# Performance work log

Hardware: AMD Instinct MI355X
Metric: run time of the kernel (lower is better)

The kernel has to match this reference:

```python
import jax, jax.numpy as jnp
import numpy as np

MAXDISP = 48


def setup_inputs() -> dict:
    key = jax.random.key(0)
    k1, k2 = jax.random.split(key)
    B, C, H, W = 4, 32, 64, 128
    x = jax.random.normal(k1, (B, C, H, W), dtype=jnp.float32)
    y = jax.random.normal(k2, (B, C, H, W), dtype=jnp.float32)
    return {"x": x, "y": y}


def reference(x, y):
    # cost[b, :C, d, h, w]   = x[b, :, h, w]     if w >= d else 0
    # cost[b, C:, d, h, w]   = y[b, :, h, w - d] if w >= d else 0
    B, C, H, W = x.shape
    D = MAXDISP
    d = jnp.arange(D)[:, None]            # [D, 1]
    w = jnp.arange(W)[None, :]            # [1, W]
    mask = (w >= d)                       # [D, W]
    mask_b = mask[None, None, :, None, :] # [1, 1, D, 1, W]

    # left features: broadcast over D, mask out w < d
    x_part = jnp.where(mask_b, x[:, :, None, :, :], 0.0)  # [B, C, D, H, W]

    # right features: gather shifted columns w - d (clipped), then mask
    y_idx = jnp.maximum(w - d, 0)                         # [D, W]
    y_g = jnp.take(y, y_idx, axis=3)                      # [B, C, H, D, W]
    y_g = jnp.transpose(y_g, (0, 1, 3, 2, 4))             # [B, C, D, H, W]
    y_part = jnp.where(mask_b, y_g, 0.0)

    return jnp.concatenate([x_part, y_part], axis=1)      # [B, 2C, D, H, W]
```

## Files before the change

### kernel.cpp

```cpp
#include <hip/hip_runtime.h>


#define CV_DSTRIDE (64 * 32)

__global__ __launch_bounds__(256) void cost_volume_kernel(
    const float* __restrict__ x, const float* __restrict__ y,
    float4* __restrict__ out)
{
    const int tid = blockIdx.x * 256 + threadIdx.x;
    const int w4 = tid & 31;
    const int h  = (tid >> 5) & 63;
    const int cc = (tid >> 11) & 63;
    const int b  = tid >> 17;
    const int w0 = w4 * 4;

    float4* outp = out + (((((b * 64 + cc) * 48) * 64 + h) * 32) + w4);

#define STORE_D(dv, e0, e1, e2, e3)                        \
    {                                                      \
        const int d_ = (dv);                               \
        float4 v;                                          \
        v.x = (w0 + 0 >= d_) ? (e0) : 0.0f;                \
        v.y = (w0 + 1 >= d_) ? (e1) : 0.0f;                \
        v.z = (w0 + 2 >= d_) ? (e2) : 0.0f;                \
        v.w = (w0 + 3 >= d_) ? (e3) : 0.0f;                \
        outp[d_ * CV_DSTRIDE] = v;                         \
    }

    if (cc < 32) {
        const float4 xv =
            *(const float4*)(x + ((b * 32 + cc) * 64 + h) * 128 + w0);
#pragma unroll
        for (int d = 0; d < 48; ++d) {
            STORE_D(d, xv.x, xv.y, xv.z, xv.w);
        }
    } else {
        float4 cur =
            *(const float4*)(y + ((b * 32 + (cc - 32)) * 64 + h) * 128 + w0);
#pragma unroll
        for (int q = 0; q < 12; ++q) {
            float4 prev;
            prev.x = __shfl_up(cur.x, 1, 32);
            prev.y = __shfl_up(cur.y, 1, 32);
            prev.z = __shfl_up(cur.z, 1, 32);
            prev.w = __shfl_up(cur.w, 1, 32);
            STORE_D(4 * q + 0, cur.x,  cur.y,  cur.z,  cur.w);
            STORE_D(4 * q + 1, prev.w, cur.x,  cur.y,  cur.z);
            STORE_D(4 * q + 2, prev.z, prev.w, cur.x,  cur.y);
            STORE_D(4 * q + 3, prev.y, prev.z, prev.w, cur.x);
            cur = prev;
        }
    }
#undef STORE_D
}

extern "C" void kernel_launch(void* const* d_in, const int* in_sizes, int n_in,
                              void* d_out, int out_size, void* d_ws, size_t ws_size,
                              hipStream_t stream) {
    const float* x = (const float*)d_in[0];
    const float* y = (const float*)d_in[1];
    float4* out = (float4*)d_out;

    const int block = 256;
    const int grid = (4 * 64 * 64 * 32) / block;
    cost_volume_kernel<<<grid, block, 0, stream>>>(x, y, out);
}
```

Baseline: 388.5 us.

## Map one thread per output float4 with contiguous nontemporal stores

Restructures the kernel so each thread writes exactly one float4 of the output and each block covers a contiguous 4 KB output chunk, with an index order that makes every block's stores sequential. It replaces the per-thread loop over 48 disparities with a variable-distance shuffle per thread, and uses nontemporal stores to keep the write-only output from polluting cache. In exchange, inputs are reloaded 48 times (mostly from cache) and the launch grows to 98304 blocks, adding index arithmetic and block scheduling overhead.

```diff
diff --git a/kernel.cpp b/kernel.cpp
--- a/kernel.cpp
+++ b/kernel.cpp
@@ -1,57 +1,57 @@
 #include <hip/hip_runtime.h>
 
 
-#define CV_DSTRIDE (64 * 32)
+typedef float f4_native __attribute__((ext_vector_type(4)));
 
 __global__ __launch_bounds__(256) void cost_volume_kernel(
     const float* __restrict__ x, const float* __restrict__ y,
-    float4* __restrict__ out)
+    f4_native* __restrict__ out)
 {
-    const int tid = blockIdx.x * 256 + threadIdx.x;
-    const int w4 = tid & 31;
-    const int h  = (tid >> 5) & 63;
-    const int cc = (tid >> 11) & 63;
-    const int b  = tid >> 17;
-    const int w0 = w4 * 4;
+    const int t    = threadIdx.x;
+    const int w4   = t & 31;
+    const int w0   = w4 << 2;
+    const int hsub = t >> 5;
 
-    float4* outp = out + (((((b * 64 + cc) * 48) * 64 + h) * 32) + w4);
+    const int g = blockIdx.x;
+    const int h = ((g & 7) << 3) + hsub;
+    int q = g >> 3;
+    const int d = q % 48;
+    q = q / 48;
+    const int cc = q & 63;
+    const int b  = q >> 6;
 
-#define STORE_D(dv, e0, e1, e2, e3)                        \
-    {                                                      \
-        const int d_ = (dv);                               \
-        float4 v;                                          \
-        v.x = (w0 + 0 >= d_) ? (e0) : 0.0f;                \
-        v.y = (w0 + 1 >= d_) ? (e1) : 0.0f;                \
-        v.z = (w0 + 2 >= d_) ? (e2) : 0.0f;                \
-        v.w = (w0 + 3 >= d_) ? (e3) : 0.0f;                \
-        outp[d_ * CV_DSTRIDE] = v;                         \
-    }
-
+    float4 v;
     if (cc < 32) {
-        const float4 xv =
-            *(const float4*)(x + ((b * 32 + cc) * 64 + h) * 128 + w0);
-#pragma unroll
-        for (int d = 0; d < 48; ++d) {
-            STORE_D(d, xv.x, xv.y, xv.z, xv.w);
-        }
+        v = *(const float4*)(x + (((b * 32 + cc) * 64 + h) << 7) + w0);
     } else {
-        float4 cur =
-            *(const float4*)(y + ((b * 32 + (cc - 32)) * 64 + h) * 128 + w0);
-#pragma unroll
-        for (int q = 0; q < 12; ++q) {
-            float4 prev;
-            prev.x = __shfl_up(cur.x, 1, 32);
-            prev.y = __shfl_up(cur.y, 1, 32);
-            prev.z = __shfl_up(cur.z, 1, 32);
-            prev.w = __shfl_up(cur.w, 1, 32);
-            STORE_D(4 * q + 0, cur.x,  cur.y,  cur.z,  cur.w);
-            STORE_D(4 * q + 1, prev.w, cur.x,  cur.y,  cur.z);
-            STORE_D(4 * q + 2, prev.z, prev.w, cur.x,  cur.y);
-            STORE_D(4 * q + 3, prev.y, prev.z, prev.w, cur.x);
-            cur = prev;
+        const float4 cur =
+            *(const float4*)(y + (((b * 32 + (cc - 32)) * 64 + h) << 7) + w0);
+        const int s = d >> 2;
+        const int r = d & 3;
+        float4 c2, p2;
+        c2.x = __shfl_up(cur.x, s, 32);
+        c2.y = __shfl_up(cur.y, s, 32);
+        c2.z = __shfl_up(cur.z, s, 32);
+        c2.w = __shfl_up(cur.w, s, 32);
+        p2.x = __shfl_up(cur.x, s + 1, 32);
+        p2.y = __shfl_up(cur.y, s + 1, 32);
+        p2.z = __shfl_up(cur.z, s + 1, 32);
+        p2.w = __shfl_up(cur.w, s + 1, 32);
+        switch (r) {
+            case 0:  v = c2; break;
+            case 1:  v = make_float4(p2.w, c2.x, c2.y, c2.z); break;
+            case 2:  v = make_float4(p2.z, p2.w, c2.x, c2.y); break;
+            default: v = make_float4(p2.y, p2.z, p2.w, c2.x); break;
         }
     }
-#undef STORE_D
+    v.x = (w0 + 0 >= d) ? v.x : 0.0f;
+    v.y = (w0 + 1 >= d) ? v.y : 0.0f;
+    v.z = (w0 + 2 >= d) ? v.z : 0.0f;
+    v.w = (w0 + 3 >= d) ? v.w : 0.0f;
+
+    f4_native vn;
+    vn.x = v.x; vn.y = v.y; vn.z = v.z; vn.w = v.w;
+    __builtin_nontemporal_store(vn, &out[g * 256 + t]);
 }
 
 extern "C" void kernel_launch(void* const* d_in, const int* in_sizes, int n_in,
@@ -59,9 +59,9 @@
                               hipStream_t stream) {
     const float* x = (const float*)d_in[0];
     const float* y = (const float*)d_in[1];
-    float4* out = (float4*)d_out;
+    f4_native* out = (f4_native*)d_out;
 
     const int block = 256;
-    const int grid = (4 * 64 * 64 * 32) / block;
+    const int grid  = 98304;
     cost_volume_kernel<<<grid, block, 0, stream>>>(x, y, out);
 }
```

Measured after the change: 429.6 us. 10.6% more time.
